# Optimization experiments

Hardware: AMD Instinct MI355X
Metric: run time of the kernel (lower is better)

## Reference

```python
import jax, jax.numpy as jnp
import numpy as np
import math

HEAD_DIM = 128
LAMBDA_INIT = 0.8


def setup_inputs() -> dict:
    key = jax.random.key(0)
    ks = jax.random.split(key, 5)
    B, H, HKV, S, D = 1, 16, 4, 2048, HEAD_DIM
    return {
        "q1": jax.random.normal(ks[0], (B, H, S, D), jnp.float32),
        "k1": jax.random.normal(ks[1], (B, HKV, S, D), jnp.float32),
        "v": jax.random.normal(ks[2], (B, HKV, S, D), jnp.float32),
        "q2": jax.random.normal(ks[3], (B, H, S, D), jnp.float32),
        "k2": jax.random.normal(ks[4], (B, HKV, S, D), jnp.float32),
        "lambda_log": jnp.full((1,), math.log(LAMBDA_INIT), jnp.float32),
    }


def _sdpa(q, k, v, scale):
    # q: [b,h,s,d]; k,v already repeated to h heads
    s = jnp.einsum("bhqd,bhkd->bhqk", q, k) * scale
    w = jax.nn.softmax(s, axis=-1)
    return jnp.einsum("bhqk,bhkd->bhqd", w, v)


def reference(q1, k1, v, q2, k2, lambda_log):
    H = q1.shape[1]
    HKV = k1.shape[1]
    rep = H // HKV
    if rep > 1:
        k1 = jnp.repeat(k1, rep, axis=1)
        k2 = jnp.repeat(k2, rep, axis=1)
        v = jnp.repeat(v, rep, axis=1)
    scale = q1.shape[-1] ** -0.5
    attn1 = _sdpa(q1, k1, v, scale)
    attn2 = _sdpa(q2, k2, v, scale)
    lam = jnp.exp(lambda_log).astype(q1.dtype)  # shape (1,), broadcasts
    return attn1 - lam * attn2
```

## Files before the change

kernel.cpp:

```cpp
#include <hip/hip_runtime.h>
#include <hip/hip_bf16.h>
#include <stdint.h>

#define D 128
#define SEQ 2048
#define NH 16
#define KVB 32
#define NTILE 64
#define BLOCK_Q 64

typedef float f32x4  __attribute__((ext_vector_type(4)));
typedef float f32x16 __attribute__((ext_vector_type(16)));
typedef short bf16x8 __attribute__((ext_vector_type(8)));

__device__ __forceinline__ unsigned cvtpk(float lo, float hi){
    unsigned r;
    asm("v_cvt_pk_bf16_f32 %0, %1, %2" : "=v"(r) : "v"(lo), "v"(hi));
    return r;
}

#define VSTRIDE 130
__global__ __launch_bounds__(256) void prep(const float* __restrict__ k1,
                                            const float* __restrict__ k2,
                                            const float* __restrict__ v,
                                            char* __restrict__ ws)
{
    __shared__ unsigned short vlds[64 * VSTRIDE];
    const int b = blockIdx.x;
    if (b < 1024){
        int cid = b * 256 + threadIdx.x;
        const float* src = (cid & 131072) ? k2 : k1;
        int r    = cid & 131071;
        int grow = r >> 4;
        int c16  = r & 15;
        const float* p = src + (size_t)grow * D + ((c16 ^ (grow & 7)) << 3);
        f32x4 a = *(const f32x4*)p;
        f32x4 c = *(const f32x4*)(p + 4);
        uint4 w;
        w.x = cvtpk(a[0], a[1]); w.y = cvtpk(a[2], a[3]);
        w.z = cvtpk(c[0], c[1]); w.w = cvtpk(c[2], c[3]);
        *(uint4*)(ws + (size_t)cid * 16) = w;
    } else {
        const int vt  = b - 1024;
        const int tid = threadIdx.x;
        const int key = tid >> 2, cg = tid & 3;
        const float* vp = v + (size_t)(vt * 64 + key) * D + cg * 32;
        #pragma unroll
        for (int i = 0; i < 8; ++i){
            f32x4 x = *(const f32x4*)(vp + i * 4);
            unsigned lo = cvtpk(x[0], x[1]);
            unsigned hi = cvtpk(x[2], x[3]);
            unsigned* dst = (unsigned*)&vlds[key * VSTRIDE + cg * 32 + i * 4];
            dst[0] = lo; dst[1] = hi;
        }
        __syncthreads();
        #pragma unroll
        for (int tt = 0; tt < 2; ++tt){
            char* outb = ws + 4194304 + (((size_t)vt * 2 + tt) << 13);
            #pragma unroll
            for (int i = 0; i < 2; ++i){
                int c = tid + 256 * i;
                int d = c >> 2;
                int s = c & 3;
                int m = tt * 32 + ((s ^ (d & 3)) << 3);
                unsigned v0 = vlds[(m + 0) * VSTRIDE + d];
                unsigned v1 = vlds[(m + 1) * VSTRIDE + d];
                unsigned v2 = vlds[(m + 2) * VSTRIDE + d];
                unsigned v3 = vlds[(m + 3) * VSTRIDE + d];
                unsigned v4 = vlds[(m + 4) * VSTRIDE + d];
                unsigned v5 = vlds[(m + 5) * VSTRIDE + d];
                unsigned v6 = vlds[(m + 6) * VSTRIDE + d];
                unsigned v7 = vlds[(m + 7) * VSTRIDE + d];
                uint4 w;
                w.x = v0 | (v1 << 16); w.y = v2 | (v3 << 16);
                w.z = v4 | (v5 << 16); w.w = v6 | (v7 << 16);
                *(uint4*)(outb + (size_t)c * 16) = w;
            }
        }
    }
}

struct Buf { char k1[8192]; char k2[8192]; char vt[8192]; };
union LdsU { Buf buf[2]; float oepi[BLOCK_Q * D]; };

__global__ __launch_bounds__(256, 2)
void diffattn(const float* __restrict__ q1, const float* __restrict__ q2,
              const float* __restrict__ ll, const char* __restrict__ ws,
              float* __restrict__ out)
{
    __shared__ LdsU lds;
    const int tid  = threadIdx.x;
    const int lane = tid & 63;
    const int wid  = tid >> 6;
    const int atn  = wid >> 1;
    const int wq   = wid & 1;
    const int g    = lane >> 5;
    const int ql   = lane & 31;

    const int bid  = blockIdx.x;
    const int sbid = (bid & 7) * 64 + (bid >> 3);
    const int qb   = sbid & 31;
    const int h    = sbid >> 5;
    const int kvh  = h >> 2;

    auto stage = [&](int bsel, int t){
        const char* b1 = ws + ((size_t)(kvh * 2048 + t * KVB) << 8);
        const char* b2 = b1 + 2097152;
        const char* bv = ws + 4194304 + ((size_t)(kvh * NTILE + t) << 13);
        char* lb = (char*)&lds.buf[bsel];
        #pragma unroll
        for (int j = 0; j < 6; ++j){
            int ci  = wid * 6 + j;
            int mat = ci >> 3, sub = ci & 7;
            const char* gb = (mat == 0) ? b1 : ((mat == 1) ? b2 : bv);
            __builtin_amdgcn_global_load_lds(
                (const __attribute__((address_space(1))) void*)(gb + (sub << 10) + (lane << 4)),
                (__attribute__((address_space(3))) void*)(lb + mat * 8192 + (sub << 10)),
                16, 0, 0);
        }
    };
    stage(0, 0);

    const float* Qbase = (atn ? q2 : q1)
        + ((size_t)h * SEQ + (size_t)qb * BLOCK_Q + wq * 32 + ql) * D;
    const float qsc = 0.08838834764831845f * 1.4426950408889634f;
    bf16x8 qf[8];
    #pragma unroll
    for (int dc = 0; dc < 8; ++dc){
        const float* p = Qbase + dc * 16 + g * 8;
        f32x4 a = *(const f32x4*)(p);
        f32x4 c = *(const f32x4*)(p + 4);
        union { bf16x8 v; unsigned u[4]; } u;
        u.u[0] = cvtpk(a[0] * qsc, a[1] * qsc);
        u.u[1] = cvtpk(a[2] * qsc, a[3] * qsc);
        u.u[2] = cvtpk(c[0] * qsc, c[1] * qsc);
        u.u[3] = cvtpk(c[2] * qsc, c[3] * qsc);
        qf[dc] = u.v;
    }

    f32x16 ot[4];
    #pragma unroll
    for (int i = 0; i < 4; ++i)
        #pragma unroll
        for (int e = 0; e < 16; ++e) ot[i][e] = 0.f;
    float mrun = 0.f, lrun = 0.f;

    __syncthreads();

    for (int t = 0; t < NTILE; ++t){
        const int cur = t & 1;
        if (t + 1 < NTILE) stage(cur ^ 1, t + 1);

        const char* kt = atn ? lds.buf[cur].k2 : lds.buf[cur].k1;
        const char* vtp = lds.buf[cur].vt;

        f32x16 st;
        const float negm = -mrun;
        #pragma unroll
        for (int e = 0; e < 16; ++e) st[e] = negm;
        const int kswz = (ql & 7) << 4;
        __builtin_amdgcn_s_setprio(1);
        #pragma unroll
        for (int dc = 0; dc < 8; ++dc){
            bf16x8 kf = *(const bf16x8*)(kt + ((ql * 256 + dc * 32 + g * 16) ^ kswz));
            st = __builtin_amdgcn_mfma_f32_32x32x16_bf16(kf, qf[dc], st, 0, 0, 0);
        }
        __builtin_amdgcn_s_setprio(0);

        float tmax = st[0];
        #pragma unroll
        for (int e = 1; e < 16; ++e) tmax = fmaxf(tmax, st[e]);
        tmax = fmaxf(tmax, __shfl_xor(tmax, 32));
        if (!__all(tmax <= 8.f)){
            float tpos = fmaxf(tmax, 0.f);
            float corr = exp2f(-tpos);
            lrun *= corr;
            #pragma unroll
            for (int i = 0; i < 4; ++i) ot[i] = ot[i] * corr;
            mrun += tpos;
            #pragma unroll
            for (int e = 0; e < 16; ++e) st[e] -= tpos;
        }
        float p[16];
        float ps = 0.f;
        #pragma unroll
        for (int e = 0; e < 16; ++e){
            float pe = exp2f(st[e]);
            p[e] = pe; ps += pe;
        }
        ps += __shfl_xor(ps, 32);
        lrun += ps;

        unsigned W[4][2];
        #pragma unroll
        for (int hh = 0; hh < 4; ++hh)
            #pragma unroll
            for (int jj = 0; jj < 2; ++jj)
                W[hh][jj] = cvtpk(p[4*hh + 2*jj], p[4*hh + 2*jj + 1]);
        bf16x8 pb[2];
        #pragma unroll
        for (int kc = 0; kc < 2; ++kc){
            unsigned a0 = W[2*kc][0],   a1 = W[2*kc][1];
            unsigned b0 = W[2*kc+1][0], b1 = W[2*kc+1][1];
            unsigned loc0 = g ? b0 : a0, loc1 = g ? b1 : a1;
            unsigned snd0 = g ? a0 : b0, snd1 = g ? a1 : b1;
            unsigned rem0 = (unsigned)__shfl_xor((int)snd0, 32);
            unsigned rem1 = (unsigned)__shfl_xor((int)snd1, 32);
            union { bf16x8 v; unsigned u[4]; } pu;
            pu.u[0] = g ? rem0 : loc0;
            pu.u[1] = g ? rem1 : loc1;
            pu.u[2] = g ? loc0 : rem0;
            pu.u[3] = g ? loc1 : rem1;
            pb[kc] = pu.v;
        }

        __builtin_amdgcn_s_setprio(1);
        #pragma unroll
        for (int db = 0; db < 4; ++db){
            const int drow = db * 32 + ql;
            #pragma unroll
            for (int kc = 0; kc < 2; ++kc){
                int s = (kc * 2 + g) ^ (drow & 3);
                bf16x8 vf = *(const bf16x8*)(vtp + drow * 64 + s * 16);
                ot[db] = __builtin_amdgcn_mfma_f32_32x32x16_bf16(vf, pb[kc], ot[db], 0, 0, 0);
            }
        }
        __builtin_amdgcn_s_setprio(0);
        __syncthreads();
    }

    const float lam = expf(ll[0]);
    const int rowl = wq * 32 + ql;
    const int eswz = (rowl & 7) << 2;

    if (atn == 1){
        const float s = -lam / lrun;
        #pragma unroll
        for (int db = 0; db < 4; ++db)
            #pragma unroll
            for (int e = 0; e < 16; ++e){
                int d = db * 32 + (e & 3) + 8 * (e >> 2) + 4 * g;
                lds.oepi[rowl * 128 + (d ^ eswz)] = ot[db][e] * s;
            }
    }
    __syncthreads();
    if (atn == 0){
        const float inv = 1.f / lrun;
        #pragma unroll
        for (int db = 0; db < 4; ++db)
            #pragma unroll
            for (int e = 0; e < 16; ++e){
                int d = db * 32 + (e & 3) + 8 * (e >> 2) + 4 * g;
                int idx = rowl * 128 + (d ^ eswz);
                lds.oepi[idx] = ot[db][e] * inv + lds.oepi[idx];
            }
    }
    __syncthreads();

    const size_t obase = ((size_t)h * SEQ + (size_t)qb * BLOCK_Q) * D;
    const int row = tid >> 2;
    const int qc  = tid & 3;
    const int sw  = (row & 7) << 2;
    #pragma unroll
    for (int j = 0; j < 8; ++j){
        int c = qc * 32 + j * 4;
        f32x4 val = *(const f32x4*)&lds.oepi[row * 128 + (c ^ sw)];
        *(f32x4*)(out + obase + (size_t)row * D + c) = val;
    }
}

extern "C" void kernel_launch(void* const* d_in, const int* in_sizes, int n_in,
                              void* d_out, int out_size, void* d_ws, size_t ws_size,
                              hipStream_t stream)
{
    (void)in_sizes; (void)n_in; (void)out_size; (void)ws_size;
    const float* q1 = (const float*)d_in[0];
    const float* k1 = (const float*)d_in[1];
    const float* v  = (const float*)d_in[2];
    const float* q2 = (const float*)d_in[3];
    const float* k2 = (const float*)d_in[4];
    const float* ll = (const float*)d_in[5];
    prep<<<1152, 256, 0, stream>>>(k1, k2, v, (char*)d_ws);
    diffattn<<<512, 256, 0, stream>>>(q1, q2, ll, (const char*)d_ws, (float*)d_out);
}
```

Before: 198.4 us.

## Load K/V fragments straight from global into registers, drop LDS staging

The prep kernel now writes K and V in the exact per-lane MFMA fragment order. The attention kernel can then load each 32-key tile directly from global memory into registers, prefetching one tile ahead, instead of staging it through double-buffered LDS with per-tile barriers. The workgroup is also halved to 128 threads with 32 query rows, so there are 1024 blocks. This removes LDS round-trips and __syncthreads from the inner loop. In exchange, KV tiles are no longer shared between the waves of a block, which roughly doubles L2/global read traffic, and load latency is exposed to per-wave scheduling.

```diff
diff --git a/kernel.cpp b/kernel.cpp
--- a/kernel.cpp
+++ b/kernel.cpp
@@ -7,7 +7,7 @@
 #define NH 16
 #define KVB 32
 #define NTILE 64
-#define BLOCK_Q 64
+#define QT 32
 
 typedef float f32x4  __attribute__((ext_vector_type(4)));
 typedef float f32x16 __attribute__((ext_vector_type(16)));
@@ -28,23 +28,28 @@
     __shared__ unsigned short vlds[64 * VSTRIDE];
     const int b = blockIdx.x;
     if (b < 1024){
-        int cid = b * 256 + threadIdx.x;
-        const float* src = (cid & 131072) ? k2 : k1;
+        int cid  = b * 256 + threadIdx.x;
+        int mat  = cid >> 17;
         int r    = cid & 131071;
         int grow = r >> 4;
-        int c16  = r & 15;
-        const float* p = src + (size_t)grow * D + ((c16 ^ (grow & 7)) << 3);
+        int dseg = r & 15;
+        const float* src = mat ? k2 : k1;
+        const float* p = src + (size_t)grow * D + dseg * 8;
         f32x4 a = *(const f32x4*)p;
         f32x4 c = *(const f32x4*)(p + 4);
         uint4 w;
         w.x = cvtpk(a[0], a[1]); w.y = cvtpk(a[2], a[3]);
         w.z = cvtpk(c[0], c[1]); w.w = cvtpk(c[2], c[3]);
-        *(uint4*)(ws + (size_t)cid * 16) = w;
+        int kvh = grow >> 11, t = (grow >> 5) & 63, key = grow & 31;
+        int dc = dseg >> 1, gh = dseg & 1;
+        char* dst = ws + (size_t)mat * 2097152
+                  + ((size_t)(kvh * 64 + t) << 13) + dc * 1024 + (gh * 32 + key) * 16;
+        *(uint4*)dst = w;
     } else {
-        const int vt  = b - 1024;
+        const int vb  = b - 1024;
         const int tid = threadIdx.x;
         const int key = tid >> 2, cg = tid & 3;
-        const float* vp = v + (size_t)(vt * 64 + key) * D + cg * 32;
+        const float* vp = v + (size_t)(vb * 64 + key) * D + cg * 32;
         #pragma unroll
         for (int i = 0; i < 8; ++i){
             f32x4 x = *(const f32x4*)(vp + i * 4);
@@ -55,74 +60,62 @@
         }
         __syncthreads();
         #pragma unroll
-        for (int tt = 0; tt < 2; ++tt){
-            char* outb = ws + 4194304 + (((size_t)vt * 2 + tt) << 13);
-            #pragma unroll
-            for (int i = 0; i < 2; ++i){
-                int c = tid + 256 * i;
-                int d = c >> 2;
-                int s = c & 3;
-                int m = tt * 32 + ((s ^ (d & 3)) << 3);
-                unsigned v0 = vlds[(m + 0) * VSTRIDE + d];
-                unsigned v1 = vlds[(m + 1) * VSTRIDE + d];
-                unsigned v2 = vlds[(m + 2) * VSTRIDE + d];
-                unsigned v3 = vlds[(m + 3) * VSTRIDE + d];
-                unsigned v4 = vlds[(m + 4) * VSTRIDE + d];
-                unsigned v5 = vlds[(m + 5) * VSTRIDE + d];
-                unsigned v6 = vlds[(m + 6) * VSTRIDE + d];
-                unsigned v7 = vlds[(m + 7) * VSTRIDE + d];
-                uint4 w;
-                w.x = v0 | (v1 << 16); w.y = v2 | (v3 << 16);
-                w.z = v4 | (v5 << 16); w.w = v6 | (v7 << 16);
-                *(uint4*)(outb + (size_t)c * 16) = w;
-            }
-        }
-    }
-}
-
-struct Buf { char k1[8192]; char k2[8192]; char vt[8192]; };
-union LdsU { Buf buf[2]; float oepi[BLOCK_Q * D]; };
-
-__global__ __launch_bounds__(256, 2)
+        for (int it = 0; it < 4; ++it){
+            int c  = tid + 256 * it;
+            int tt = c >> 9;
+            int cc = c & 511;
+            int r  = cc >> 6;
+            int l  = cc & 63;
+            int db = r >> 1, kc = r & 1;
+            int m  = tt * 32 + kc * 16 + (l >> 5) * 8;
+            int dd = db * 32 + (l & 31);
+            unsigned v0 = vlds[(m + 0) * VSTRIDE + dd];
+            unsigned v1 = vlds[(m + 1) * VSTRIDE + dd];
+            unsigned v2 = vlds[(m + 2) * VSTRIDE + dd];
+            unsigned v3 = vlds[(m + 3) * VSTRIDE + dd];
+            unsigned v4 = vlds[(m + 4) * VSTRIDE + dd];
+            unsigned v5 = vlds[(m + 5) * VSTRIDE + dd];
+            unsigned v6 = vlds[(m + 6) * VSTRIDE + dd];
+            unsigned v7 = vlds[(m + 7) * VSTRIDE + dd];
+            uint4 w;
+            w.x = v0 | (v1 << 16); w.y = v2 | (v3 << 16);
+            w.z = v4 | (v5 << 16); w.w = v6 | (v7 << 16);
+            char* dst = ws + 4194304 + ((size_t)(vb * 2 + tt) << 13) + r * 1024 + l * 16;
+            *(uint4*)dst = w;
+        }
+    }
+}
+
+__global__ __launch_bounds__(128, 2)
 void diffattn(const float* __restrict__ q1, const float* __restrict__ q2,
               const float* __restrict__ ll, const char* __restrict__ ws,
               float* __restrict__ out)
 {
-    __shared__ LdsU lds;
+    __shared__ float oepi[QT * D];
     const int tid  = threadIdx.x;
     const int lane = tid & 63;
-    const int wid  = tid >> 6;
-    const int atn  = wid >> 1;
-    const int wq   = wid & 1;
+    const int atn  = tid >> 6;
     const int g    = lane >> 5;
     const int ql   = lane & 31;
 
     const int bid  = blockIdx.x;
-    const int sbid = (bid & 7) * 64 + (bid >> 3);
-    const int qb   = sbid & 31;
-    const int h    = sbid >> 5;
+    const int sbid = (bid & 7) * 128 + (bid >> 3);
+    const int qb   = sbid & 63;
+    const int h    = sbid >> 6;
     const int kvh  = h >> 2;
 
-    auto stage = [&](int bsel, int t){
-        const char* b1 = ws + ((size_t)(kvh * 2048 + t * KVB) << 8);
-        const char* b2 = b1 + 2097152;
-        const char* bv = ws + 4194304 + ((size_t)(kvh * NTILE + t) << 13);
-        char* lb = (char*)&lds.buf[bsel];
-        #pragma unroll
-        for (int j = 0; j < 6; ++j){
-            int ci  = wid * 6 + j;
-            int mat = ci >> 3, sub = ci & 7;
-            const char* gb = (mat == 0) ? b1 : ((mat == 1) ? b2 : bv);
-            __builtin_amdgcn_global_load_lds(
-                (const __attribute__((address_space(1))) void*)(gb + (sub << 10) + (lane << 4)),
-                (__attribute__((address_space(3))) void*)(lb + mat * 8192 + (sub << 10)),
-                16, 0, 0);
-        }
-    };
-    stage(0, 0);
+    const char* kbase = ws + (size_t)atn * 2097152 + ((size_t)(kvh * 64) << 13);
+    const char* vbase = ws + 4194304 + ((size_t)(kvh * 64) << 13);
+    const int loff = lane * 16;
+
+    bf16x8 ak[8], av[8];
+    #pragma unroll
+    for (int r = 0; r < 8; ++r) ak[r] = *(const bf16x8*)(kbase + r * 1024 + loff);
+    #pragma unroll
+    for (int r = 0; r < 8; ++r) av[r] = *(const bf16x8*)(vbase + r * 1024 + loff);
 
     const float* Qbase = (atn ? q2 : q1)
-        + ((size_t)h * SEQ + (size_t)qb * BLOCK_Q + wq * 32 + ql) * D;
+        + ((size_t)h * SEQ + (size_t)qb * QT + ql) * D;
     const float qsc = 0.08838834764831845f * 1.4426950408889634f;
     bf16x8 qf[8];
     #pragma unroll
@@ -145,27 +138,24 @@
         for (int e = 0; e < 16; ++e) ot[i][e] = 0.f;
     float mrun = 0.f, lrun = 0.f;
 
-    __syncthreads();
-
     for (int t = 0; t < NTILE; ++t){
-        const int cur = t & 1;
-        if (t + 1 < NTILE) stage(cur ^ 1, t + 1);
-
-        const char* kt = atn ? lds.buf[cur].k2 : lds.buf[cur].k1;
-        const char* vtp = lds.buf[cur].vt;
+        const int tn = (t + 1 < NTILE) ? t + 1 : t;
 
         f32x16 st;
         const float negm = -mrun;
         #pragma unroll
         for (int e = 0; e < 16; ++e) st[e] = negm;
-        const int kswz = (ql & 7) << 4;
         __builtin_amdgcn_s_setprio(1);
         #pragma unroll
-        for (int dc = 0; dc < 8; ++dc){
-            bf16x8 kf = *(const bf16x8*)(kt + ((ql * 256 + dc * 32 + g * 16) ^ kswz));
-            st = __builtin_amdgcn_mfma_f32_32x32x16_bf16(kf, qf[dc], st, 0, 0, 0);
-        }
+        for (int dc = 0; dc < 8; ++dc)
+            st = __builtin_amdgcn_mfma_f32_32x32x16_bf16(ak[dc], qf[dc], st, 0, 0, 0);
         __builtin_amdgcn_s_setprio(0);
+
+        {
+            const char* kp = kbase + ((size_t)tn << 13);
+            #pragma unroll
+            for (int r = 0; r < 8; ++r) ak[r] = *(const bf16x8*)(kp + r * 1024 + loff);
+        }
 
         float tmax = st[0];
         #pragma unroll
@@ -217,21 +207,20 @@
         __builtin_amdgcn_s_setprio(1);
         #pragma unroll
         for (int db = 0; db < 4; ++db){
-            const int drow = db * 32 + ql;
-            #pragma unroll
-            for (int kc = 0; kc < 2; ++kc){
-                int s = (kc * 2 + g) ^ (drow & 3);
-                bf16x8 vf = *(const bf16x8*)(vtp + drow * 64 + s * 16);
-                ot[db] = __builtin_amdgcn_mfma_f32_32x32x16_bf16(vf, pb[kc], ot[db], 0, 0, 0);
-            }
+            ot[db] = __builtin_amdgcn_mfma_f32_32x32x16_bf16(av[db*2+0], pb[0], ot[db], 0, 0, 0);
+            ot[db] = __builtin_amdgcn_mfma_f32_32x32x16_bf16(av[db*2+1], pb[1], ot[db], 0, 0, 0);
         }
         __builtin_amdgcn_s_setprio(0);
-        __syncthreads();
+
+        {
+            const char* vp = vbase + ((size_t)tn << 13);
+            #pragma unroll
+            for (int r = 0; r < 8; ++r) av[r] = *(const bf16x8*)(vp + r * 1024 + loff);
+        }
     }
 
     const float lam = expf(ll[0]);
-    const int rowl = wq * 32 + ql;
-    const int eswz = (rowl & 7) << 2;
+    const int eswz = (ql & 7) << 2;
 
     if (atn == 1){
         const float s = -lam / lrun;
@@ -240,7 +229,7 @@
             #pragma unroll
             for (int e = 0; e < 16; ++e){
                 int d = db * 32 + (e & 3) + 8 * (e >> 2) + 4 * g;
-                lds.oepi[rowl * 128 + (d ^ eswz)] = ot[db][e] * s;
+                oepi[ql * 128 + (d ^ eswz)] = ot[db][e] * s;
             }
     }
     __syncthreads();
@@ -251,20 +240,20 @@
             #pragma unroll
             for (int e = 0; e < 16; ++e){
                 int d = db * 32 + (e & 3) + 8 * (e >> 2) + 4 * g;
-                int idx = rowl * 128 + (d ^ eswz);
-                lds.oepi[idx] = ot[db][e] * inv + lds.oepi[idx];
+                int idx = ql * 128 + (d ^ eswz);
+                oepi[idx] = ot[db][e] * inv + oepi[idx];
             }
     }
     __syncthreads();
 
-    const size_t obase = ((size_t)h * SEQ + (size_t)qb * BLOCK_Q) * D;
+    const size_t obase = ((size_t)h * SEQ + (size_t)qb * QT) * D;
     const int row = tid >> 2;
     const int qc  = tid & 3;
     const int sw  = (row & 7) << 2;
     #pragma unroll
     for (int j = 0; j < 8; ++j){
         int c = qc * 32 + j * 4;
-        f32x4 val = *(const f32x4*)&lds.oepi[row * 128 + (c ^ sw)];
+        f32x4 val = *(const f32x4*)&oepi[row * 128 + (c ^ sw)];
         *(f32x4*)(out + obase + (size_t)row * D + c) = val;
     }
 }
@@ -281,5 +270,5 @@
     const float* k2 = (const float*)d_in[4];
     const float* ll = (const float*)d_in[5];
     prep<<<1152, 256, 0, stream>>>(k1, k2, v, (char*)d_ws);
-    diffattn<<<512, 256, 0, stream>>>(q1, q2, ll, (const char*)d_ws, (float*)d_out);
-}
+    diffattn<<<1024, 128, 0, stream>>>(q1, q2, ll, (const char*)d_ws, (float*)d_out);
+}
```

After: 188.4 us. -5.0%, faster.
